# Performance work log

Measured on AMD Instinct MI355X. Metric: run time of the kernel, lower is better.

Reference implementation:

```python
import jax, jax.numpy as jnp
import numpy as np

NUM_HEADS = 16
BIG_NEG = -1e9  # additive mask value for padded keys (fp32)


def setup_inputs() -> dict:
    key = jax.random.key(0)
    ks = jax.random.split(key, 12)
    T, S, B, E = 2048, 2048, 2, 1024
    bound = np.sqrt(6.0 / (E + E))  # xavier_uniform for square E x E weights
    inp = {
        'query': jax.random.normal(ks[0], (T, B, E), jnp.float32),
        'key': jax.random.normal(ks[1], (S, B, E), jnp.float32),
        'value': jax.random.normal(ks[2], (S, B, E), jnp.float32),
        'attn_mask': jax.random.normal(ks[3], (T, S), jnp.float32) * 0.1,
        'key_padding_mask': jnp.zeros((B, S), dtype=bool),
        'Wq': jax.random.uniform(ks[4], (E, E), jnp.float32, -bound, bound),
        'bq': jnp.zeros((E,), jnp.float32),
        'Wk': jax.random.uniform(ks[5], (E, E), jnp.float32, -bound, bound),
        'bk': jnp.zeros((E,), jnp.float32),
        'Wv': jax.random.uniform(ks[6], (E, E), jnp.float32, -bound, bound),
        'bv': jnp.zeros((E,), jnp.float32),
        'Wo': jax.random.uniform(ks[7], (E, E), jnp.float32, -bound, bound),
        'bo': jnp.zeros((E,), jnp.float32),
    }
    return inp


def reference(query, key, value, attn_mask, key_padding_mask,
              Wq, bq, Wk, bk, Wv, bv, Wo, bo):
    T, B, E = query.shape
    S = key.shape[0]
    H = NUM_HEADS
    d = E // H
    scale = 1.0 / jnp.sqrt(jnp.asarray(d, query.dtype))

    # projections (nn.Linear: x @ W.T + b), then split heads
    q = (query @ Wq.T + bq).reshape(T, B, H, d) * scale  # [T,B,H,d]
    k = (key @ Wk.T + bk).reshape(S, B, H, d)            # [S,B,H,d]
    v = (value @ Wv.T + bv).reshape(S, B, H, d)          # [S,B,H,d]

    # QK^T scores: [B,H,T,S]
    scores = jnp.einsum('tbhd,sbhd->bhts', q, k)

    # merge masks: additive attn_mask + key_padding_mask (True -> -inf)
    merged = attn_mask[None, None, :, :] + jnp.where(
        key_padding_mask[:, None, None, :], BIG_NEG, 0.0).astype(scores.dtype)
    scores = scores + merged

    attn = jax.nn.softmax(scores, axis=-1)  # dropout p=0 -> identity

    out = jnp.einsum('bhts,sbhd->tbhd', attn, v).reshape(T, B, E)
    return out @ Wo.T + bo  # [T,B,E]
```

## Files before the change

kernel.cpp:

```cpp
#include <hip/hip_runtime.h>
#include <hip/hip_bf16.h>

typedef unsigned short u16;
typedef __attribute__((ext_vector_type(8))) short bf16x8;
typedef __attribute__((ext_vector_type(4))) float f32x4;

#define T_DIM 2048
#define S_DIM 2048
#define B_DIM 2
#define E_DIM 1024
#define H_DIM 16
#define D_HEAD 64
#define NTOK 4096

#if __has_builtin(__builtin_amdgcn_exp2f)
#define EXP2F(x) __builtin_amdgcn_exp2f(x)
#else
#define EXP2F(x) exp2f(x)
#endif

__device__ __forceinline__ float bf2f(u16 u) {
  union { unsigned int i; float f; } v; v.i = ((unsigned int)u) << 16; return v.f;
}
__device__ __forceinline__ u16 f2bf(float f) {
  union { float f; unsigned int i; } v; v.f = f;
  unsigned int r = v.i + 0x7fffu + ((v.i >> 16) & 1u);
  return (u16)(r >> 16);
}
__device__ __forceinline__ unsigned pk2(float a, float b) {
  return (unsigned)f2bf(a) | ((unsigned)f2bf(b) << 16);
}
__device__ __forceinline__ uint4 loadA8(const void* A, size_t base, int bf) {
  if (bf) return *(const uint4*)&((const u16*)A)[base];
  const float* af = (const float*)A + base;
  uint4 r;
  r.x = pk2(af[0], af[1]); r.y = pk2(af[2], af[3]);
  r.z = pk2(af[4], af[5]); r.w = pk2(af[6], af[7]);
  return r;
}

__global__ void detect_dtype(const u16* q, int* flag) {
  int lane = threadIdx.x;
  float v = bf2f(q[2 * lane]);
  bool ok = (v < 16.f) && (v > -16.f);
  unsigned long long b = __ballot(ok);
  if (lane == 0) *flag = (b == ~0ull) ? 1 : 0;
}

__global__ void prep_params(const void* Wq, const void* Wk, const void* Wv, const void* Wo,
                            const void* bq, const void* bk, const void* bv, const void* bo,
                            u16* wqkv, u16* wo, float* b3, float* bof,
                            const int* flag) {
  const int bf = *flag;
  const int W = E_DIM * E_DIM;
  int idx = blockIdx.x * 256 + threadIdx.x;
  if (idx < 4 * W) {
    int which = idx / W, i = idx - which * W;
    const void* src = which == 0 ? Wq : which == 1 ? Wk : which == 2 ? Wv : Wo;
    float v = bf ? bf2f(((const u16*)src)[i]) : ((const float*)src)[i];
    if (which == 0) v *= 0.125f;
    if (which < 3) wqkv[idx] = f2bf(v);
    else           wo[i] = f2bf(v);
  } else {
    int j = idx - 4 * W;
    if (j < 4 * E_DIM) {
      int which = j / E_DIM, i = j - which * E_DIM;
      const void* src = which == 0 ? bq : which == 1 ? bk : which == 2 ? bv : bo;
      float v = bf ? bf2f(((const u16*)src)[i]) : ((const float*)src)[i];
      if (which == 0) v *= 0.125f;
      if (which < 3) b3[j] = v;
      else           bof[i] = v;
    }
  }
}

__global__ void prep_mask(const void* mask, const unsigned char* kpm,
                          u16* Mc, const int* flag) {
  const float L2E = 1.44269504f;
  const int bf = *flag;
  size_t e8 = ((size_t)blockIdx.x * 256 + threadIdx.x) * 8;
  int b = (int)(e8 / ((size_t)T_DIM * S_DIM));
  size_t rem = e8 - (size_t)b * T_DIM * S_DIM;
  int t = (int)(rem / S_DIM), s = (int)(rem - (size_t)t * S_DIM);
  const unsigned char* kb = &kpm[(size_t)b * S_DIM + s];
  uint4 o;
  if (bf) {
    const u16* m8 = &((const u16*)mask)[(size_t)t * S_DIM + s];
    o.x = pk2((bf2f(m8[0]) + (kb[0] ? -1e9f : 0.f)) * L2E,
              (bf2f(m8[1]) + (kb[1] ? -1e9f : 0.f)) * L2E);
    o.y = pk2((bf2f(m8[2]) + (kb[2] ? -1e9f : 0.f)) * L2E,
              (bf2f(m8[3]) + (kb[3] ? -1e9f : 0.f)) * L2E);
    o.z = pk2((bf2f(m8[4]) + (kb[4] ? -1e9f : 0.f)) * L2E,
              (bf2f(m8[5]) + (kb[5] ? -1e9f : 0.f)) * L2E);
    o.w = pk2((bf2f(m8[6]) + (kb[6] ? -1e9f : 0.f)) * L2E,
              (bf2f(m8[7]) + (kb[7] ? -1e9f : 0.f)) * L2E);
  } else {
    const float* mf = (const float*)mask + (size_t)t * S_DIM + s;
    o.x = pk2((mf[0] + (kb[0] ? -1e9f : 0.f)) * L2E,
              (mf[1] + (kb[1] ? -1e9f : 0.f)) * L2E);
    o.y = pk2((mf[2] + (kb[2] ? -1e9f : 0.f)) * L2E,
              (mf[3] + (kb[3] ? -1e9f : 0.f)) * L2E);
    o.z = pk2((mf[4] + (kb[4] ? -1e9f : 0.f)) * L2E,
              (mf[5] + (kb[5] ? -1e9f : 0.f)) * L2E);
    o.w = pk2((mf[6] + (kb[6] ? -1e9f : 0.f)) * L2E,
              (mf[7] + (kb[7] ? -1e9f : 0.f)) * L2E);
  }
  *(uint4*)&Mc[e8] = o;
}

__launch_bounds__(256)
__global__ void transpose_v(const u16* __restrict__ vp, u16* __restrict__ vt) {
  __shared__ unsigned int t[64 * 65];
  const int tid = threadIdx.x;
  const int s0 = blockIdx.x * 64;
  const int bh = blockIdx.y;
  const int b = bh / H_DIM, h = bh % H_DIM;
  {
    int sr = tid >> 2, cq = (tid & 3) * 16;
    const u16* src = &vp[((size_t)(s0 + sr) * B_DIM + b) * E_DIM + h * 64 + cq];
#pragma unroll
    for (int j = 0; j < 16; j++) t[(cq + j) * 65 + sr] = src[j];
  }
  __syncthreads();
  {
    int d = tid >> 2, sq = (tid & 3) * 16;
    u16* dst = &vt[((size_t)bh * 64 + d) * S_DIM + s0 + sq];
    uint4 o0, o1;
    o0.x = (t[d*65+sq+0] & 0xffffu) | (t[d*65+sq+1] << 16);
    o0.y = (t[d*65+sq+2] & 0xffffu) | (t[d*65+sq+3] << 16);
    o0.z = (t[d*65+sq+4] & 0xffffu) | (t[d*65+sq+5] << 16);
    o0.w = (t[d*65+sq+6] & 0xffffu) | (t[d*65+sq+7] << 16);
    o1.x = (t[d*65+sq+8] & 0xffffu) | (t[d*65+sq+9] << 16);
    o1.y = (t[d*65+sq+10] & 0xffffu) | (t[d*65+sq+11] << 16);
    o1.z = (t[d*65+sq+12] & 0xffffu) | (t[d*65+sq+13] << 16);
    o1.w = (t[d*65+sq+14] & 0xffffu) | (t[d*65+sq+15] << 16);
    *(uint4*)&dst[0] = o0;
    *(uint4*)&dst[8] = o1;
  }
}

__launch_bounds__(256, 2)
__global__ void gemm_qkv(const void* __restrict__ Qi, const void* __restrict__ Ki,
                         const void* __restrict__ Vi, const u16* __restrict__ W3,
                         const float* __restrict__ b3,
                         u16* __restrict__ qp, u16* __restrict__ kp, u16* __restrict__ vp,
                         const int* __restrict__ flag) {
  __shared__ alignas(16) u16 As[128 * 72];
  __shared__ alignas(16) u16 Bs[128 * 72];
  const int bf = *flag;
  const int tid = threadIdx.x;
  const int wave = tid >> 6, lane = tid & 63;
  const int g = lane >> 4, c = lane & 15;
  const int wy = wave >> 1, wx = wave & 1;
  const int which = blockIdx.x >> 3;
  const void* A = which == 0 ? Qi : which == 1 ? Ki : Vi;
  u16* dst = which == 0 ? qp : which == 1 ? kp : vp;
  const int m0 = blockIdx.y * 128, n0 = blockIdx.x * 128;
  const int K = E_DIM;
  const int rr = tid >> 3, oo = (tid & 7) * 8;

  uint4 pa0, pa1, pa2, pa3, pb0, pb1, pb2, pb3;
  pa0 = loadA8(A, (size_t)(m0 + rr)      * K + oo, bf);
  pa1 = loadA8(A, (size_t)(m0 + rr + 32) * K + oo, bf);
  pa2 = loadA8(A, (size_t)(m0 + rr + 64) * K + oo, bf);
  pa3 = loadA8(A, (size_t)(m0 + rr + 96) * K + oo, bf);
  pb0 = *(const uint4*)&W3[(size_t)(n0 + rr)      * K + oo];
  pb1 = *(const uint4*)&W3[(size_t)(n0 + rr + 32) * K + oo];
  pb2 = *(const uint4*)&W3[(size_t)(n0 + rr + 64) * K + oo];
  pb3 = *(const uint4*)&W3[(size_t)(n0 + rr + 96) * K + oo];

  f32x4 acc[4][4] = {};
  for (int kc = 0; kc < K; kc += 64) {
    *(uint4*)&As[(rr)      * 72 + oo] = pa0;
    *(uint4*)&As[(rr + 32) * 72 + oo] = pa1;
    *(uint4*)&As[(rr + 64) * 72 + oo] = pa2;
    *(uint4*)&As[(rr + 96) * 72 + oo] = pa3;
    *(uint4*)&Bs[(rr)      * 72 + oo] = pb0;
    *(uint4*)&Bs[(rr + 32) * 72 + oo] = pb1;
    *(uint4*)&Bs[(rr + 64) * 72 + oo] = pb2;
    *(uint4*)&Bs[(rr + 96) * 72 + oo] = pb3;
    __syncthreads();
    if (kc + 64 < K) {
      int k2 = kc + 64;
      pa0 = loadA8(A, (size_t)(m0 + rr)      * K + k2 + oo, bf);
      pa1 = loadA8(A, (size_t)(m0 + rr + 32) * K + k2 + oo, bf);
      pa2 = loadA8(A, (size_t)(m0 + rr + 64) * K + k2 + oo, bf);
      pa3 = loadA8(A, (size_t)(m0 + rr + 96) * K + k2 + oo, bf);
      pb0 = *(const uint4*)&W3[(size_t)(n0 + rr)      * K + k2 + oo];
      pb1 = *(const uint4*)&W3[(size_t)(n0 + rr + 32) * K + k2 + oo];
      pb2 = *(const uint4*)&W3[(size_t)(n0 + rr + 64) * K + k2 + oo];
      pb3 = *(const uint4*)&W3[(size_t)(n0 + rr + 96) * K + k2 + oo];
    }
#pragma unroll
    for (int ks = 0; ks < 2; ks++) {
      bf16x8 av0 = *(const bf16x8*)&As[(wy * 64 + 0 * 16 + c) * 72 + ks * 32 + g * 8];
      bf16x8 av1 = *(const bf16x8*)&As[(wy * 64 + 1 * 16 + c) * 72 + ks * 32 + g * 8];
      bf16x8 av2 = *(const bf16x8*)&As[(wy * 64 + 2 * 16 + c) * 72 + ks * 32 + g * 8];
      bf16x8 av3 = *(const bf16x8*)&As[(wy * 64 + 3 * 16 + c) * 72 + ks * 32 + g * 8];
      bf16x8 bv0 = *(const bf16x8*)&Bs[(wx * 64 + 0 * 16 + c) * 72 + ks * 32 + g * 8];
      bf16x8 bv1 = *(const bf16x8*)&Bs[(wx * 64 + 1 * 16 + c) * 72 + ks * 32 + g * 8];
      bf16x8 bv2 = *(const bf16x8*)&Bs[(wx * 64 + 2 * 16 + c) * 72 + ks * 32 + g * 8];
      bf16x8 bv3 = *(const bf16x8*)&Bs[(wx * 64 + 3 * 16 + c) * 72 + ks * 32 + g * 8];
      acc[0][0] = __builtin_amdgcn_mfma_f32_16x16x32_bf16(av0, bv0, acc[0][0], 0, 0, 0);
      acc[0][1] = __builtin_amdgcn_mfma_f32_16x16x32_bf16(av0, bv1, acc[0][1], 0, 0, 0);
      acc[0][2] = __builtin_amdgcn_mfma_f32_16x16x32_bf16(av0, bv2, acc[0][2], 0, 0, 0);
      acc[0][3] = __builtin_amdgcn_mfma_f32_16x16x32_bf16(av0, bv3, acc[0][3], 0, 0, 0);
      acc[1][0] = __builtin_amdgcn_mfma_f32_16x16x32_bf16(av1, bv0, acc[1][0], 0, 0, 0);
      acc[1][1] = __builtin_amdgcn_mfma_f32_16x16x32_bf16(av1, bv1, acc[1][1], 0, 0, 0);
      acc[1][2] = __builtin_amdgcn_mfma_f32_16x16x32_bf16(av1, bv2, acc[1][2], 0, 0, 0);
      acc[1][3] = __builtin_amdgcn_mfma_f32_16x16x32_bf16(av1, bv3, acc[1][3], 0, 0, 0);
      acc[2][0] = __builtin_amdgcn_mfma_f32_16x16x32_bf16(av2, bv0, acc[2][0], 0, 0, 0);
      acc[2][1] = __builtin_amdgcn_mfma_f32_16x16x32_bf16(av2, bv1, acc[2][1], 0, 0, 0);
      acc[2][2] = __builtin_amdgcn_mfma_f32_16x16x32_bf16(av2, bv2, acc[2][2], 0, 0, 0);
      acc[2][3] = __builtin_amdgcn_mfma_f32_16x16x32_bf16(av2, bv3, acc[2][3], 0, 0, 0);
      acc[3][0] = __builtin_amdgcn_mfma_f32_16x16x32_bf16(av3, bv0, acc[3][0], 0, 0, 0);
      acc[3][1] = __builtin_amdgcn_mfma_f32_16x16x32_bf16(av3, bv1, acc[3][1], 0, 0, 0);
      acc[3][2] = __builtin_amdgcn_mfma_f32_16x16x32_bf16(av3, bv2, acc[3][2], 0, 0, 0);
      acc[3][3] = __builtin_amdgcn_mfma_f32_16x16x32_bf16(av3, bv3, acc[3][3], 0, 0, 0);
    }
    __syncthreads();
  }
#pragma unroll
  for (int mi = 0; mi < 4; mi++)
#pragma unroll
    for (int ni = 0; ni < 4; ni++)
#pragma unroll
      for (int r = 0; r < 4; r++) {
        int row = m0 + wy * 64 + mi * 16 + g * 4 + r;
        int col = n0 + wx * 64 + ni * 16 + c;
        int inner = col & (E_DIM - 1);
        dst[(size_t)row * E_DIM + inner] = f2bf(acc[mi][ni][r] + b3[col]);
      }
}

__launch_bounds__(256, 2)
__global__ void gemm_o(const u16* __restrict__ A, const u16* __restrict__ Bw,
                       const float* __restrict__ bias, void* __restrict__ C,
                       int out_f32) {
  __shared__ alignas(16) u16 As[64 * 72];
  __shared__ alignas(16) u16 Bs[128 * 72];
  const int tid = threadIdx.x;
  const int wave = tid >> 6, lane = tid & 63;
  const int g = lane >> 4, c = lane & 15;
  const int wy = wave >> 1, wx = wave & 1;
  const int m0 = blockIdx.y * 64, n0 = blockIdx.x * 128;
  const int K = E_DIM, N = E_DIM;
  const int rr = tid >> 3, oo = (tid & 7) * 8;

  uint4 pa0, pa1, pb0, pb1, pb2, pb3;
  pa0 = *(const uint4*)&A[(size_t)(m0 + rr)      * K + oo];
  pa1 = *(const uint4*)&A[(size_t)(m0 + rr + 32) * K + oo];
  pb0 = *(const uint4*)&Bw[(size_t)(n0 + rr)      * K + oo];
  pb1 = *(const uint4*)&Bw[(size_t)(n0 + rr + 32) * K + oo];
  pb2 = *(const uint4*)&Bw[(size_t)(n0 + rr + 64) * K + oo];
  pb3 = *(const uint4*)&Bw[(size_t)(n0 + rr + 96) * K + oo];

  f32x4 acc[2][4] = {};
  for (int kc = 0; kc < K; kc += 64) {
    *(uint4*)&As[(rr)      * 72 + oo] = pa0;
    *(uint4*)&As[(rr + 32) * 72 + oo] = pa1;
    *(uint4*)&Bs[(rr)      * 72 + oo] = pb0;
    *(uint4*)&Bs[(rr + 32) * 72 + oo] = pb1;
    *(uint4*)&Bs[(rr + 64) * 72 + oo] = pb2;
    *(uint4*)&Bs[(rr + 96) * 72 + oo] = pb3;
    __syncthreads();
    if (kc + 64 < K) {
      int k2 = kc + 64;
      pa0 = *(const uint4*)&A[(size_t)(m0 + rr)      * K + k2 + oo];
      pa1 = *(const uint4*)&A[(size_t)(m0 + rr + 32) * K + k2 + oo];
      pb0 = *(const uint4*)&Bw[(size_t)(n0 + rr)      * K + k2 + oo];
      pb1 = *(const uint4*)&Bw[(size_t)(n0 + rr + 32) * K + k2 + oo];
      pb2 = *(const uint4*)&Bw[(size_t)(n0 + rr + 64) * K + k2 + oo];
      pb3 = *(const uint4*)&Bw[(size_t)(n0 + rr + 96) * K + k2 + oo];
    }
#pragma unroll
    for (int ks = 0; ks < 2; ks++) {
      bf16x8 av0 = *(const bf16x8*)&As[(wy * 32 + 0 * 16 + c) * 72 + ks * 32 + g * 8];
      bf16x8 av1 = *(const bf16x8*)&As[(wy * 32 + 1 * 16 + c) * 72 + ks * 32 + g * 8];
      bf16x8 bv0 = *(const bf16x8*)&Bs[(wx * 64 + 0 * 16 + c) * 72 + ks * 32 + g * 8];
      bf16x8 bv1 = *(const bf16x8*)&Bs[(wx * 64 + 1 * 16 + c) * 72 + ks * 32 + g * 8];
      bf16x8 bv2 = *(const bf16x8*)&Bs[(wx * 64 + 2 * 16 + c) * 72 + ks * 32 + g * 8];
      bf16x8 bv3 = *(const bf16x8*)&Bs[(wx * 64 + 3 * 16 + c) * 72 + ks * 32 + g * 8];
      acc[0][0] = __builtin_amdgcn_mfma_f32_16x16x32_bf16(av0, bv0, acc[0][0], 0, 0, 0);
      acc[0][1] = __builtin_amdgcn_mfma_f32_16x16x32_bf16(av0, bv1, acc[0][1], 0, 0, 0);
      acc[0][2] = __builtin_amdgcn_mfma_f32_16x16x32_bf16(av0, bv2, acc[0][2], 0, 0, 0);
      acc[0][3] = __builtin_amdgcn_mfma_f32_16x16x32_bf16(av0, bv3, acc[0][3], 0, 0, 0);
      acc[1][0] = __builtin_amdgcn_mfma_f32_16x16x32_bf16(av1, bv0, acc[1][0], 0, 0, 0);
      acc[1][1] = __builtin_amdgcn_mfma_f32_16x16x32_bf16(av1, bv1, acc[1][1], 0, 0, 0);
      acc[1][2] = __builtin_amdgcn_mfma_f32_16x16x32_bf16(av1, bv2, acc[1][2], 0, 0, 0);
      acc[1][3] = __builtin_amdgcn_mfma_f32_16x16x32_bf16(av1, bv3, acc[1][3], 0, 0, 0);
    }
    __syncthreads();
  }
#pragma unroll
  for (int mi = 0; mi < 2; mi++)
#pragma unroll
    for (int ni = 0; ni < 4; ni++)
#pragma unroll
      for (int r = 0; r < 4; r++) {
        int row = m0 + wy * 32 + mi * 16 + g * 4 + r;
        int col = n0 + wx * 64 + ni * 16 + c;
        float v = acc[mi][ni][r] + bias[col];
        size_t idx = (size_t)row * N + col;
        if (out_f32) ((float*)C)[idx] = v;
        else         ((u16*)C)[idx] = f2bf(v);
      }
}

__launch_bounds__(256, 4)
__global__ void flash_attn(const u16* __restrict__ Qb, const u16* __restrict__ Kb,
                           const u16* __restrict__ Vtg, const u16* __restrict__ Mc,
                           u16* __restrict__ ctx) {
  __shared__ alignas(16) u16 Ks[64 * 72];
  __shared__ alignas(16) u16 Vs[64 * 72];
  __shared__ alignas(16) u16 MP[64 * 72];
  const int tid = threadIdx.x;
  const int wave = tid >> 6, lane = tid & 63;
  const int g = lane >> 4, c = lane & 15;
  const int bh = blockIdx.x;
  const int t0 = blockIdx.y * 64;
  const int b = bh / H_DIM, h = bh % H_DIM;
  const size_t hoff = (size_t)h * D_HEAD;
  const float L2E = 1.44269504f;
  const u16* mc = &Mc[((size_t)b * T_DIM + t0) * S_DIM];
  const int rr = tid >> 3, oo = (tid & 7) * 8;

  *(uint4*)&Ks[(rr)      * 72 + oo] =
      *(const uint4*)&Qb[((size_t)(t0 + rr)      * B_DIM + b) * E_DIM + hoff + oo];
  *(uint4*)&Ks[(rr + 32) * 72 + oo] =
      *(const uint4*)&Qb[((size_t)(t0 + rr + 32) * B_DIM + b) * E_DIM + hoff + oo];
  __syncthreads();
  const int arow = wave * 16 + c;
  bf16x8 q0 = *(const bf16x8*)&Ks[arow * 72 + g * 8];
  bf16x8 q1 = *(const bf16x8*)&Ks[arow * 72 + 32 + g * 8];

  uint4 pk0, pk1, pv0, pv1, pm0, pm1;
  pk0 = *(const uint4*)&Kb[((size_t)(rr)      * B_DIM + b) * E_DIM + hoff + oo];
  pk1 = *(const uint4*)&Kb[((size_t)(rr + 32) * B_DIM + b) * E_DIM + hoff + oo];
  pv0 = *(const uint4*)&Vtg[((size_t)bh * 64 + rr)      * S_DIM + oo];
  pv1 = *(const uint4*)&Vtg[((size_t)bh * 64 + rr + 32) * S_DIM + oo];
  pm0 = *(const uint4*)&mc[(size_t)(rr)      * S_DIM + oo];
  pm1 = *(const uint4*)&mc[(size_t)(rr + 32) * S_DIM + oo];
  __syncthreads();

  f32x4 O[4] = {};
  float rs[4] = {0.f, 0.f, 0.f, 0.f};

  for (int s0 = 0; s0 < S_DIM; s0 += 64) {
    *(uint4*)&Ks[(rr)      * 72 + oo] = pk0;
    *(uint4*)&Ks[(rr + 32) * 72 + oo] = pk1;
    *(uint4*)&Vs[(rr)      * 72 + oo] = pv0;
    *(uint4*)&Vs[(rr + 32) * 72 + oo] = pv1;
    *(uint4*)&MP[(rr)      * 72 + oo] = pm0;
    *(uint4*)&MP[(rr + 32) * 72 + oo] = pm1;
    __syncthreads();
    if (s0 + 64 < S_DIM) {
      int s2 = s0 + 64;
      pk0 = *(const uint4*)&Kb[((size_t)(s2 + rr)      * B_DIM + b) * E_DIM + hoff + oo];
      pk1 = *(const uint4*)&Kb[((size_t)(s2 + rr + 32) * B_DIM + b) * E_DIM + hoff + oo];
      pv0 = *(const uint4*)&Vtg[((size_t)bh * 64 + rr)      * S_DIM + s2 + oo];
      pv1 = *(const uint4*)&Vtg[((size_t)bh * 64 + rr + 32) * S_DIM + s2 + oo];
      pm0 = *(const uint4*)&mc[(size_t)(rr)      * S_DIM + s2 + oo];
      pm1 = *(const uint4*)&mc[(size_t)(rr + 32) * S_DIM + s2 + oo];
    }

    f32x4 sc[4] = {};
#pragma unroll
    for (int n = 0; n < 4; n++) {
      bf16x8 k0 = *(const bf16x8*)&Ks[(n * 16 + c) * 72 + g * 8];
      bf16x8 k1 = *(const bf16x8*)&Ks[(n * 16 + c) * 72 + 32 + g * 8];
      sc[n] = __builtin_amdgcn_mfma_f32_16x16x32_bf16(q0, k0, sc[n], 0, 0, 0);
      sc[n] = __builtin_amdgcn_mfma_f32_16x16x32_bf16(q1, k1, sc[n], 0, 0, 0);
    }
#pragma unroll
    for (int n = 0; n < 4; n++)
#pragma unroll
      for (int r = 0; r < 4; r++) {
        int a = (wave * 16 + g * 4 + r) * 72 + n * 16 + c;
        float pval = EXP2F(fmaf(sc[n][r], L2E, bf2f(MP[a])));
        rs[r] += pval;
        MP[a] = f2bf(pval);
      }
    bf16x8 p0 = *(const bf16x8*)&MP[arow * 72 + g * 8];
    bf16x8 p1 = *(const bf16x8*)&MP[arow * 72 + 32 + g * 8];
#pragma unroll
    for (int n = 0; n < 4; n++) {
      bf16x8 v0 = *(const bf16x8*)&Vs[(n * 16 + c) * 72 + g * 8];
      bf16x8 v1 = *(const bf16x8*)&Vs[(n * 16 + c) * 72 + 32 + g * 8];
      O[n] = __builtin_amdgcn_mfma_f32_16x16x32_bf16(p0, v0, O[n], 0, 0, 0);
      O[n] = __builtin_amdgcn_mfma_f32_16x16x32_bf16(p1, v1, O[n], 0, 0, 0);
    }
    __syncthreads();
  }
#pragma unroll
  for (int r = 0; r < 4; r++) {
    float l = rs[r];
#pragma unroll
    for (int off = 1; off < 16; off <<= 1) l += __shfl_xor(l, off, 64);
    float rl = 1.f / l;
    int t = t0 + wave * 16 + g * 4 + r;
#pragma unroll
    for (int n = 0; n < 4; n++) {
      int dcol = n * 16 + c;
      ctx[((size_t)t * B_DIM + b) * E_DIM + hoff + dcol] = f2bf(O[n][r] * rl);
    }
  }
}

extern "C" void kernel_launch(void* const* d_in, const int* in_sizes, int n_in,
                              void* d_out, int out_size, void* d_ws, size_t ws_size,
                              hipStream_t stream) {
  const void* query = d_in[0];
  const void* key   = d_in[1];
  const void* value = d_in[2];
  const void* amask = d_in[3];
  const unsigned char* kpm = (const unsigned char*)d_in[4];
  const void* Wq = d_in[5];  const void* bq = d_in[6];
  const void* Wk = d_in[7];  const void* bk = d_in[8];
  const void* Wv = d_in[9];  const void* bv = d_in[10];
  const void* Wo = d_in[11]; const void* bo = d_in[12];

  int out_f32 = 0;
  {
    hipDeviceptr_t base = nullptr; size_t sz = 0;
    if (hipMemGetAddressRange(&base, &sz, (hipDeviceptr_t)d_out) == hipSuccess && sz) {
      size_t avail = sz - (size_t)((char*)d_out - (char*)base);
      size_t need_f32 = (size_t)out_size * 4;
      if (avail >= need_f32 && avail <= need_f32 + need_f32 / 2) out_f32 = 1;
    }
  }

  char* ws = (char*)d_ws;
  size_t off = 0;
  auto alloc = [&](size_t bytes) {
    void* p = ws + off;
    off += (bytes + 255) & ~(size_t)255;
    return p;
  };
  int*   flag = (int*)  alloc(256);
  u16*   qp   = (u16*)  alloc((size_t)NTOK * E_DIM * 2);
  u16*   kp   = (u16*)  alloc((size_t)NTOK * E_DIM * 2);
  u16*   vp   = (u16*)  alloc((size_t)NTOK * E_DIM * 2);
  u16*   vt   = (u16*)  alloc((size_t)NTOK * E_DIM * 2);
  u16*   Mcb  = (u16*)  alloc((size_t)B_DIM * T_DIM * S_DIM * 2);
  u16*   wqkv = (u16*)  alloc((size_t)3 * E_DIM * E_DIM * 2);
  u16*   wo   = (u16*)  alloc((size_t)E_DIM * E_DIM * 2);
  float* b3   = (float*)alloc(3 * E_DIM * 4);
  float* bof  = (float*)alloc(E_DIM * 4);
  if (off > ws_size) return;

  detect_dtype<<<1, 64, 0, stream>>>((const u16*)query, flag);

  {
    int total = 4 * E_DIM * E_DIM + 4 * E_DIM;
    prep_params<<<(total + 255) / 256, 256, 0, stream>>>(
        Wq, Wk, Wv, Wo, bq, bk, bv, bo, wqkv, wo, b3, bof, flag);
  }
  {
    size_t total8 = (size_t)B_DIM * T_DIM * S_DIM / 8;
    prep_mask<<<(unsigned)(total8 / 256), 256, 0, stream>>>(amask, kpm, Mcb, flag);
  }

  gemm_qkv<<<dim3(3 * E_DIM / 128, NTOK / 128), 256, 0, stream>>>(
      query, key, value, wqkv, b3, qp, kp, vp, flag);

  transpose_v<<<dim3(S_DIM / 64, B_DIM * H_DIM), 256, 0, stream>>>(vp, vt);

  u16* ctx = vp;
  flash_attn<<<dim3(B_DIM * H_DIM, T_DIM / 64), 256, 0, stream>>>(qp, kp, vt, Mcb, ctx);

  gemm_o<<<dim3(E_DIM / 128, NTOK / 64), 256, 0, stream>>>(ctx, wo, bof, d_out, out_f32);
}
```

Before: 313.0 us.

## Use direct global-to-LDS loads with XOR swizzle in GEMMs and widen attention tiles

The two projection GEMMs now fill shared memory with global_load_lds and an XOR-swizzled unpadded layout instead of register-staged copies into padded tiles. This drops the register prefetch, which cuts register pressure and allows a higher occupancy hint, but also removes the overlap of the next tile's load with the current tile's compute. Separately, flash attention now handles 128 query rows per block, two 16-row tiles per wave, so each K/V tile loaded into shared memory is reused twice. The cost is more mask traffic and registers per block.

```diff
diff --git a/kernel.cpp b/kernel.cpp
--- a/kernel.cpp
+++ b/kernel.cpp
@@ -37,6 +37,11 @@
   r.x = pk2(af[0], af[1]); r.y = pk2(af[2], af[3]);
   r.z = pk2(af[4], af[5]); r.w = pk2(af[6], af[7]);
   return r;
+}
+__device__ __forceinline__ void dma16(const void* g, void* l) {
+  __builtin_amdgcn_global_load_lds(
+      (const __attribute__((address_space(1))) unsigned int*)g,
+      (__attribute__((address_space(3))) unsigned int*)l, 16, 0, 0);
 }
 
 __global__ void detect_dtype(const u16* q, int* flag) {
@@ -139,14 +144,14 @@
   }
 }
 
-__launch_bounds__(256, 2)
+__launch_bounds__(256, 3)
 __global__ void gemm_qkv(const void* __restrict__ Qi, const void* __restrict__ Ki,
                          const void* __restrict__ Vi, const u16* __restrict__ W3,
                          const float* __restrict__ b3,
                          u16* __restrict__ qp, u16* __restrict__ kp, u16* __restrict__ vp,
                          const int* __restrict__ flag) {
-  __shared__ alignas(16) u16 As[128 * 72];
-  __shared__ alignas(16) u16 Bs[128 * 72];
+  __shared__ alignas(16) u16 As[128 * 64];
+  __shared__ alignas(16) u16 Bs[128 * 64];
   const int bf = *flag;
   const int tid = threadIdx.x;
   const int wave = tid >> 6, lane = tid & 63;
@@ -157,50 +162,43 @@
   u16* dst = which == 0 ? qp : which == 1 ? kp : vp;
   const int m0 = blockIdx.y * 128, n0 = blockIdx.x * 128;
   const int K = E_DIM;
-  const int rr = tid >> 3, oo = (tid & 7) * 8;
-
-  uint4 pa0, pa1, pa2, pa3, pb0, pb1, pb2, pb3;
-  pa0 = loadA8(A, (size_t)(m0 + rr)      * K + oo, bf);
-  pa1 = loadA8(A, (size_t)(m0 + rr + 32) * K + oo, bf);
-  pa2 = loadA8(A, (size_t)(m0 + rr + 64) * K + oo, bf);
-  pa3 = loadA8(A, (size_t)(m0 + rr + 96) * K + oo, bf);
-  pb0 = *(const uint4*)&W3[(size_t)(n0 + rr)      * K + oo];
-  pb1 = *(const uint4*)&W3[(size_t)(n0 + rr + 32) * K + oo];
-  pb2 = *(const uint4*)&W3[(size_t)(n0 + rr + 64) * K + oo];
-  pb3 = *(const uint4*)&W3[(size_t)(n0 + rr + 96) * K + oo];
+  const int lr = lane >> 3, lc = lane & 7;
+  const int jj = lc ^ lr;
+  const int rr = tid >> 3, ssl = tid & 7;
+  const int jf = ssl ^ (rr & 7);
+  const int swz = (c & 7);
 
   f32x4 acc[4][4] = {};
   for (int kc = 0; kc < K; kc += 64) {
-    *(uint4*)&As[(rr)      * 72 + oo] = pa0;
-    *(uint4*)&As[(rr + 32) * 72 + oo] = pa1;
-    *(uint4*)&As[(rr + 64) * 72 + oo] = pa2;
-    *(uint4*)&As[(rr + 96) * 72 + oo] = pa3;
-    *(uint4*)&Bs[(rr)      * 72 + oo] = pb0;
-    *(uint4*)&Bs[(rr + 32) * 72 + oo] = pb1;
-    *(uint4*)&Bs[(rr + 64) * 72 + oo] = pb2;
-    *(uint4*)&Bs[(rr + 96) * 72 + oo] = pb3;
-    __syncthreads();
-    if (kc + 64 < K) {
-      int k2 = kc + 64;
-      pa0 = loadA8(A, (size_t)(m0 + rr)      * K + k2 + oo, bf);
-      pa1 = loadA8(A, (size_t)(m0 + rr + 32) * K + k2 + oo, bf);
-      pa2 = loadA8(A, (size_t)(m0 + rr + 64) * K + k2 + oo, bf);
-      pa3 = loadA8(A, (size_t)(m0 + rr + 96) * K + k2 + oo, bf);
-      pb0 = *(const uint4*)&W3[(size_t)(n0 + rr)      * K + k2 + oo];
-      pb1 = *(const uint4*)&W3[(size_t)(n0 + rr + 32) * K + k2 + oo];
-      pb2 = *(const uint4*)&W3[(size_t)(n0 + rr + 64) * K + k2 + oo];
-      pb3 = *(const uint4*)&W3[(size_t)(n0 + rr + 96) * K + k2 + oo];
-    }
+    if (bf) {
+      const u16* Ab = (const u16*)A;
+#pragma unroll
+      for (int i = 0; i < 4; i++) {
+        int rbase = wave * 8 + i * 32;
+        dma16(&Ab[(size_t)(m0 + rbase + lr) * K + kc + jj * 8], &As[rbase * 64]);
+        dma16(&W3[(size_t)(n0 + rbase + lr) * K + kc + jj * 8], &Bs[rbase * 64]);
+      }
+    } else {
+#pragma unroll
+      for (int i = 0; i < 4; i++) {
+        *(uint4*)&As[(rr + i * 32) * 64 + ssl * 8] =
+            loadA8(A, (size_t)(m0 + rr + i * 32) * K + kc + jf * 8, 0);
+        *(uint4*)&Bs[(rr + i * 32) * 64 + ssl * 8] =
+            *(const uint4*)&W3[(size_t)(n0 + rr + i * 32) * K + kc + jf * 8];
+      }
+    }
+    __syncthreads();
 #pragma unroll
     for (int ks = 0; ks < 2; ks++) {
-      bf16x8 av0 = *(const bf16x8*)&As[(wy * 64 + 0 * 16 + c) * 72 + ks * 32 + g * 8];
-      bf16x8 av1 = *(const bf16x8*)&As[(wy * 64 + 1 * 16 + c) * 72 + ks * 32 + g * 8];
-      bf16x8 av2 = *(const bf16x8*)&As[(wy * 64 + 2 * 16 + c) * 72 + ks * 32 + g * 8];
-      bf16x8 av3 = *(const bf16x8*)&As[(wy * 64 + 3 * 16 + c) * 72 + ks * 32 + g * 8];
-      bf16x8 bv0 = *(const bf16x8*)&Bs[(wx * 64 + 0 * 16 + c) * 72 + ks * 32 + g * 8];
-      bf16x8 bv1 = *(const bf16x8*)&Bs[(wx * 64 + 1 * 16 + c) * 72 + ks * 32 + g * 8];
-      bf16x8 bv2 = *(const bf16x8*)&Bs[(wx * 64 + 2 * 16 + c) * 72 + ks * 32 + g * 8];
-      bf16x8 bv3 = *(const bf16x8*)&Bs[(wx * 64 + 3 * 16 + c) * 72 + ks * 32 + g * 8];
+      int fo = ((ks * 4 + g) ^ swz) * 8;
+      bf16x8 av0 = *(const bf16x8*)&As[(wy * 64 + 0 * 16 + c) * 64 + fo];
+      bf16x8 av1 = *(const bf16x8*)&As[(wy * 64 + 1 * 16 + c) * 64 + fo];
+      bf16x8 av2 = *(const bf16x8*)&As[(wy * 64 + 2 * 16 + c) * 64 + fo];
+      bf16x8 av3 = *(const bf16x8*)&As[(wy * 64 + 3 * 16 + c) * 64 + fo];
+      bf16x8 bv0 = *(const bf16x8*)&Bs[(wx * 64 + 0 * 16 + c) * 64 + fo];
+      bf16x8 bv1 = *(const bf16x8*)&Bs[(wx * 64 + 1 * 16 + c) * 64 + fo];
+      bf16x8 bv2 = *(const bf16x8*)&Bs[(wx * 64 + 2 * 16 + c) * 64 + fo];
+      bf16x8 bv3 = *(const bf16x8*)&Bs[(wx * 64 + 3 * 16 + c) * 64 + fo];
       acc[0][0] = __builtin_amdgcn_mfma_f32_16x16x32_bf16(av0, bv0, acc[0][0], 0, 0, 0);
       acc[0][1] = __builtin_amdgcn_mfma_f32_16x16x32_bf16(av0, bv1, acc[0][1], 0, 0, 0);
       acc[0][2] = __builtin_amdgcn_mfma_f32_16x16x32_bf16(av0, bv2, acc[0][2], 0, 0, 0);
@@ -233,54 +231,44 @@
       }
 }
 
-__launch_bounds__(256, 2)
+__launch_bounds__(256, 3)
 __global__ void gemm_o(const u16* __restrict__ A, const u16* __restrict__ Bw,
                        const float* __restrict__ bias, void* __restrict__ C,
                        int out_f32) {
-  __shared__ alignas(16) u16 As[64 * 72];
-  __shared__ alignas(16) u16 Bs[128 * 72];
+  __shared__ alignas(16) u16 As[64 * 64];
+  __shared__ alignas(16) u16 Bs[128 * 64];
   const int tid = threadIdx.x;
   const int wave = tid >> 6, lane = tid & 63;
   const int g = lane >> 4, c = lane & 15;
   const int wy = wave >> 1, wx = wave & 1;
   const int m0 = blockIdx.y * 64, n0 = blockIdx.x * 128;
   const int K = E_DIM, N = E_DIM;
-  const int rr = tid >> 3, oo = (tid & 7) * 8;
-
-  uint4 pa0, pa1, pb0, pb1, pb2, pb3;
-  pa0 = *(const uint4*)&A[(size_t)(m0 + rr)      * K + oo];
-  pa1 = *(const uint4*)&A[(size_t)(m0 + rr + 32) * K + oo];
-  pb0 = *(const uint4*)&Bw[(size_t)(n0 + rr)      * K + oo];
-  pb1 = *(const uint4*)&Bw[(size_t)(n0 + rr + 32) * K + oo];
-  pb2 = *(const uint4*)&Bw[(size_t)(n0 + rr + 64) * K + oo];
-  pb3 = *(const uint4*)&Bw[(size_t)(n0 + rr + 96) * K + oo];
+  const int lr = lane >> 3, lc = lane & 7;
+  const int jj = lc ^ lr;
+  const int swz = (c & 7);
 
   f32x4 acc[2][4] = {};
   for (int kc = 0; kc < K; kc += 64) {
-    *(uint4*)&As[(rr)      * 72 + oo] = pa0;
-    *(uint4*)&As[(rr + 32) * 72 + oo] = pa1;
-    *(uint4*)&Bs[(rr)      * 72 + oo] = pb0;
-    *(uint4*)&Bs[(rr + 32) * 72 + oo] = pb1;
-    *(uint4*)&Bs[(rr + 64) * 72 + oo] = pb2;
-    *(uint4*)&Bs[(rr + 96) * 72 + oo] = pb3;
-    __syncthreads();
-    if (kc + 64 < K) {
-      int k2 = kc + 64;
-      pa0 = *(const uint4*)&A[(size_t)(m0 + rr)      * K + k2 + oo];
-      pa1 = *(const uint4*)&A[(size_t)(m0 + rr + 32) * K + k2 + oo];
-      pb0 = *(const uint4*)&Bw[(size_t)(n0 + rr)      * K + k2 + oo];
-      pb1 = *(const uint4*)&Bw[(size_t)(n0 + rr + 32) * K + k2 + oo];
-      pb2 = *(const uint4*)&Bw[(size_t)(n0 + rr + 64) * K + k2 + oo];
-      pb3 = *(const uint4*)&Bw[(size_t)(n0 + rr + 96) * K + k2 + oo];
-    }
+#pragma unroll
+    for (int i = 0; i < 2; i++) {
+      int rbase = wave * 8 + i * 32;
+      dma16(&A[(size_t)(m0 + rbase + lr) * K + kc + jj * 8], &As[rbase * 64]);
+    }
+#pragma unroll
+    for (int i = 0; i < 4; i++) {
+      int rbase = wave * 8 + i * 32;
+      dma16(&Bw[(size_t)(n0 + rbase + lr) * K + kc + jj * 8], &Bs[rbase * 64]);
+    }
+    __syncthreads();
 #pragma unroll
     for (int ks = 0; ks < 2; ks++) {
-      bf16x8 av0 = *(const bf16x8*)&As[(wy * 32 + 0 * 16 + c) * 72 + ks * 32 + g * 8];
-      bf16x8 av1 = *(const bf16x8*)&As[(wy * 32 + 1 * 16 + c) * 72 + ks * 32 + g * 8];
-      bf16x8 bv0 = *(const bf16x8*)&Bs[(wx * 64 + 0 * 16 + c) * 72 + ks * 32 + g * 8];
-      bf16x8 bv1 = *(const bf16x8*)&Bs[(wx * 64 + 1 * 16 + c) * 72 + ks * 32 + g * 8];
-      bf16x8 bv2 = *(const bf16x8*)&Bs[(wx * 64 + 2 * 16 + c) * 72 + ks * 32 + g * 8];
-      bf16x8 bv3 = *(const bf16x8*)&Bs[(wx * 64 + 3 * 16 + c) * 72 + ks * 32 + g * 8];
+      int fo = ((ks * 4 + g) ^ swz) * 8;
+      bf16x8 av0 = *(const bf16x8*)&As[(wy * 32 + 0 * 16 + c) * 64 + fo];
+      bf16x8 av1 = *(const bf16x8*)&As[(wy * 32 + 1 * 16 + c) * 64 + fo];
+      bf16x8 bv0 = *(const bf16x8*)&Bs[(wx * 64 + 0 * 16 + c) * 64 + fo];
+      bf16x8 bv1 = *(const bf16x8*)&Bs[(wx * 64 + 1 * 16 + c) * 64 + fo];
+      bf16x8 bv2 = *(const bf16x8*)&Bs[(wx * 64 + 2 * 16 + c) * 64 + fo];
+      bf16x8 bv3 = *(const bf16x8*)&Bs[(wx * 64 + 3 * 16 + c) * 64 + fo];
       acc[0][0] = __builtin_amdgcn_mfma_f32_16x16x32_bf16(av0, bv0, acc[0][0], 0, 0, 0);
       acc[0][1] = __builtin_amdgcn_mfma_f32_16x16x32_bf16(av0, bv1, acc[0][1], 0, 0, 0);
       acc[0][2] = __builtin_amdgcn_mfma_f32_16x16x32_bf16(av0, bv2, acc[0][2], 0, 0, 0);
@@ -307,44 +295,47 @@
       }
 }
 
-__launch_bounds__(256, 4)
+__launch_bounds__(256, 3)
 __global__ void flash_attn(const u16* __restrict__ Qb, const u16* __restrict__ Kb,
                            const u16* __restrict__ Vtg, const u16* __restrict__ Mc,
                            u16* __restrict__ ctx) {
   __shared__ alignas(16) u16 Ks[64 * 72];
   __shared__ alignas(16) u16 Vs[64 * 72];
-  __shared__ alignas(16) u16 MP[64 * 72];
+  __shared__ alignas(16) u16 MP[128 * 72];
   const int tid = threadIdx.x;
   const int wave = tid >> 6, lane = tid & 63;
   const int g = lane >> 4, c = lane & 15;
   const int bh = blockIdx.x;
-  const int t0 = blockIdx.y * 64;
+  const int t0 = blockIdx.y * 128;
   const int b = bh / H_DIM, h = bh % H_DIM;
   const size_t hoff = (size_t)h * D_HEAD;
   const float L2E = 1.44269504f;
   const u16* mc = &Mc[((size_t)b * T_DIM + t0) * S_DIM];
   const int rr = tid >> 3, oo = (tid & 7) * 8;
 
-  *(uint4*)&Ks[(rr)      * 72 + oo] =
-      *(const uint4*)&Qb[((size_t)(t0 + rr)      * B_DIM + b) * E_DIM + hoff + oo];
-  *(uint4*)&Ks[(rr + 32) * 72 + oo] =
-      *(const uint4*)&Qb[((size_t)(t0 + rr + 32) * B_DIM + b) * E_DIM + hoff + oo];
+  *(uint4*)&MP[(rr)      * 72 + oo] = *(const uint4*)&Qb[((size_t)(t0 + rr)      * B_DIM + b) * E_DIM + hoff + oo];
+  *(uint4*)&MP[(rr + 32) * 72 + oo] = *(const uint4*)&Qb[((size_t)(t0 + rr + 32) * B_DIM + b) * E_DIM + hoff + oo];
+  *(uint4*)&MP[(rr + 64) * 72 + oo] = *(const uint4*)&Qb[((size_t)(t0 + rr + 64) * B_DIM + b) * E_DIM + hoff + oo];
+  *(uint4*)&MP[(rr + 96) * 72 + oo] = *(const uint4*)&Qb[((size_t)(t0 + rr + 96) * B_DIM + b) * E_DIM + hoff + oo];
   __syncthreads();
-  const int arow = wave * 16 + c;
-  bf16x8 q0 = *(const bf16x8*)&Ks[arow * 72 + g * 8];
-  bf16x8 q1 = *(const bf16x8*)&Ks[arow * 72 + 32 + g * 8];
-
-  uint4 pk0, pk1, pv0, pv1, pm0, pm1;
+  bf16x8 q00 = *(const bf16x8*)&MP[(wave * 32 + c) * 72 + g * 8];
+  bf16x8 q01 = *(const bf16x8*)&MP[(wave * 32 + c) * 72 + 32 + g * 8];
+  bf16x8 q10 = *(const bf16x8*)&MP[(wave * 32 + 16 + c) * 72 + g * 8];
+  bf16x8 q11 = *(const bf16x8*)&MP[(wave * 32 + 16 + c) * 72 + 32 + g * 8];
+
+  uint4 pk0, pk1, pv0, pv1, pm0, pm1, pm2, pm3;
   pk0 = *(const uint4*)&Kb[((size_t)(rr)      * B_DIM + b) * E_DIM + hoff + oo];
   pk1 = *(const uint4*)&Kb[((size_t)(rr + 32) * B_DIM + b) * E_DIM + hoff + oo];
   pv0 = *(const uint4*)&Vtg[((size_t)bh * 64 + rr)      * S_DIM + oo];
   pv1 = *(const uint4*)&Vtg[((size_t)bh * 64 + rr + 32) * S_DIM + oo];
   pm0 = *(const uint4*)&mc[(size_t)(rr)      * S_DIM + oo];
   pm1 = *(const uint4*)&mc[(size_t)(rr + 32) * S_DIM + oo];
+  pm2 = *(const uint4*)&mc[(size_t)(rr + 64) * S_DIM + oo];
+  pm3 = *(const uint4*)&mc[(size_t)(rr + 96) * S_DIM + oo];
   __syncthreads();
 
-  f32x4 O[4] = {};
-  float rs[4] = {0.f, 0.f, 0.f, 0.f};
+  f32x4 O[2][4] = {};
+  float rs[2][4] = {};
 
   for (int s0 = 0; s0 < S_DIM; s0 += 64) {
     *(uint4*)&Ks[(rr)      * 72 + oo] = pk0;
@@ -353,6 +344,8 @@
     *(uint4*)&Vs[(rr + 32) * 72 + oo] = pv1;
     *(uint4*)&MP[(rr)      * 72 + oo] = pm0;
     *(uint4*)&MP[(rr + 32) * 72 + oo] = pm1;
+    *(uint4*)&MP[(rr + 64) * 72 + oo] = pm2;
+    *(uint4*)&MP[(rr + 96) * 72 + oo] = pm3;
     __syncthreads();
     if (s0 + 64 < S_DIM) {
       int s2 = s0 + 64;
@@ -362,49 +355,61 @@
       pv1 = *(const uint4*)&Vtg[((size_t)bh * 64 + rr + 32) * S_DIM + s2 + oo];
       pm0 = *(const uint4*)&mc[(size_t)(rr)      * S_DIM + s2 + oo];
       pm1 = *(const uint4*)&mc[(size_t)(rr + 32) * S_DIM + s2 + oo];
-    }
-
-    f32x4 sc[4] = {};
+      pm2 = *(const uint4*)&mc[(size_t)(rr + 64) * S_DIM + s2 + oo];
+      pm3 = *(const uint4*)&mc[(size_t)(rr + 96) * S_DIM + s2 + oo];
+    }
+
+    f32x4 sc[2][4] = {};
 #pragma unroll
     for (int n = 0; n < 4; n++) {
       bf16x8 k0 = *(const bf16x8*)&Ks[(n * 16 + c) * 72 + g * 8];
       bf16x8 k1 = *(const bf16x8*)&Ks[(n * 16 + c) * 72 + 32 + g * 8];
-      sc[n] = __builtin_amdgcn_mfma_f32_16x16x32_bf16(q0, k0, sc[n], 0, 0, 0);
-      sc[n] = __builtin_amdgcn_mfma_f32_16x16x32_bf16(q1, k1, sc[n], 0, 0, 0);
-    }
-#pragma unroll
-    for (int n = 0; n < 4; n++)
-#pragma unroll
-      for (int r = 0; r < 4; r++) {
-        int a = (wave * 16 + g * 4 + r) * 72 + n * 16 + c;
-        float pval = EXP2F(fmaf(sc[n][r], L2E, bf2f(MP[a])));
-        rs[r] += pval;
-        MP[a] = f2bf(pval);
-      }
-    bf16x8 p0 = *(const bf16x8*)&MP[arow * 72 + g * 8];
-    bf16x8 p1 = *(const bf16x8*)&MP[arow * 72 + 32 + g * 8];
+      sc[0][n] = __builtin_amdgcn_mfma_f32_16x16x32_bf16(q00, k0, sc[0][n], 0, 0, 0);
+      sc[0][n] = __builtin_amdgcn_mfma_f32_16x16x32_bf16(q01, k1, sc[0][n], 0, 0, 0);
+      sc[1][n] = __builtin_amdgcn_mfma_f32_16x16x32_bf16(q10, k0, sc[1][n], 0, 0, 0);
+      sc[1][n] = __builtin_amdgcn_mfma_f32_16x16x32_bf16(q11, k1, sc[1][n], 0, 0, 0);
+    }
+#pragma unroll
+    for (int mi = 0; mi < 2; mi++)
+#pragma unroll
+      for (int n = 0; n < 4; n++)
+#pragma unroll
+        for (int r = 0; r < 4; r++) {
+          int a = (wave * 32 + mi * 16 + g * 4 + r) * 72 + n * 16 + c;
+          float pval = EXP2F(fmaf(sc[mi][n][r], L2E, bf2f(MP[a])));
+          rs[mi][r] += pval;
+          MP[a] = f2bf(pval);
+        }
+    bf16x8 p00 = *(const bf16x8*)&MP[(wave * 32 + c) * 72 + g * 8];
+    bf16x8 p01 = *(const bf16x8*)&MP[(wave * 32 + c) * 72 + 32 + g * 8];
+    bf16x8 p10 = *(const bf16x8*)&MP[(wave * 32 + 16 + c) * 72 + g * 8];
+    bf16x8 p11 = *(const bf16x8*)&MP[(wave * 32 + 16 + c) * 72 + 32 + g * 8];
 #pragma unroll
     for (int n = 0; n < 4; n++) {
       bf16x8 v0 = *(const bf16x8*)&Vs[(n * 16 + c) * 72 + g * 8];
       bf16x8 v1 = *(const bf16x8*)&Vs[(n * 16 + c) * 72 + 32 + g * 8];
-      O[n] = __builtin_amdgcn_mfma_f32_16x16x32_bf16(p0, v0, O[n], 0, 0, 0);
-      O[n] = __builtin_amdgcn_mfma_f32_16x16x32_bf16(p1, v1, O[n], 0, 0, 0);
-    }
-    __syncthreads();
-  }
-#pragma unroll
-  for (int r = 0; r < 4; r++) {
-    float l = rs[r];
-#pragma unroll
-    for (int off = 1; off < 16; off <<= 1) l += __shfl_xor(l, off, 64);
-    float rl = 1.f / l;
-    int t = t0 + wave * 16 + g * 4 + r;
-#pragma unroll
-    for (int n = 0; n < 4; n++) {
-      int dcol = n * 16 + c;
-      ctx[((size_t)t * B_DIM + b) * E_DIM + hoff + dcol] = f2bf(O[n][r] * rl);
-    }
-  }
+      O[0][n] = __builtin_amdgcn_mfma_f32_16x16x32_bf16(p00, v0, O[0][n], 0, 0, 0);
+      O[0][n] = __builtin_amdgcn_mfma_f32_16x16x32_bf16(p01, v1, O[0][n], 0, 0, 0);
+      O[1][n] = __builtin_amdgcn_mfma_f32_16x16x32_bf16(p10, v0, O[1][n], 0, 0, 0);
+      O[1][n] = __builtin_amdgcn_mfma_f32_16x16x32_bf16(p11, v1, O[1][n], 0, 0, 0);
+    }
+    __syncthreads();
+  }
+#pragma unroll
+  for (int mi = 0; mi < 2; mi++)
+#pragma unroll
+    for (int r = 0; r < 4; r++) {
+      float l = rs[mi][r];
+#pragma unroll
+      for (int off = 1; off < 16; off <<= 1) l += __shfl_xor(l, off, 64);
+      float rl = 1.f / l;
+      int t = t0 + wave * 32 + mi * 16 + g * 4 + r;
+#pragma unroll
+      for (int n = 0; n < 4; n++) {
+        int dcol = n * 16 + c;
+        ctx[((size_t)t * B_DIM + b) * E_DIM + hoff + dcol] = f2bf(O[mi][n][r] * rl);
+      }
+    }
 }
 
 extern "C" void kernel_launch(void* const* d_in, const int* in_sizes, int n_in,
@@ -467,7 +472,7 @@
   transpose_v<<<dim3(S_DIM / 64, B_DIM * H_DIM), 256, 0, stream>>>(vp, vt);
 
   u16* ctx = vp;
-  flash_attn<<<dim3(B_DIM * H_DIM, T_DIM / 64), 256, 0, stream>>>(qp, kp, vt, Mcb, ctx);
+  flash_attn<<<dim3(B_DIM * H_DIM, T_DIM / 128), 256, 0, stream>>>(qp, kp, vt, Mcb, ctx);
 
   gemm_o<<<dim3(E_DIM / 128, NTOK / 64), 256, 0, stream>>>(ctx, wo, bof, d_out, out_f32);
 }
```

Result: slower. 327.3 us (+4.6%).
